# Kernel tuning notes

Hardware: AMD Instinct MI355X
Metric: run time of the kernel (lower is better)

## Reference

```python
import jax, jax.numpy as jnp
import numpy as np

TOP_K = 2

def setup_inputs() -> dict:
    key = jax.random.key(0)
    k1, k2, k3, k4 = jax.random.split(key, 4)
    B, S, H, E, F = 2, 1024, 1024, 16, 1024
    hidden_states = jax.random.normal(k1, (B, S, H), dtype=jnp.float32)
    router_w = jax.random.normal(k2, (H, E), dtype=jnp.float32) * 0.02
    w_gate_up = jax.random.normal(k3, (E, H, 2 * F), dtype=jnp.float32) * 0.02
    w_down = jax.random.normal(k4, (E, F, H), dtype=jnp.float32) * 0.02
    return {"hidden_states": hidden_states, "router_w": router_w,
            "w_gate_up": w_gate_up, "w_down": w_down}

def reference(hidden_states, router_w, w_gate_up, w_down):
    B, S, H = hidden_states.shape
    E = router_w.shape[-1]
    flat = hidden_states.reshape(-1, H)                      # [T, H]
    T = flat.shape[0]
    # Routing: topk_then_softmax (default softmax_order)
    logits = flat @ router_w                                 # [T, E]
    top_vals, top_idx = jax.lax.top_k(logits, TOP_K)         # [T, K]
    routing_weights = jax.nn.softmax(top_vals, axis=-1)      # [T, K]
    # Scatter routing weights into a dense combine matrix [T, E]
    combine = jnp.zeros((T, E), dtype=flat.dtype)
    combine = combine.at[jnp.arange(T)[:, None], top_idx].add(routing_weights)
    # Fused expert FFN (per _FusedExpertTemplate, act_fn = SiLU-gated)
    gu = jnp.einsum('th,ehf->etf', flat, w_gate_up)          # [E, T, 2F]
    gate, up = jnp.split(gu, 2, axis=-1)
    gated = jax.nn.silu(gate) * up                           # [E, T, F]
    expert_out = jnp.einsum('etf,efh->eth', gated, w_down)   # [E, T, H]
    out = jnp.einsum('eth,te->th', expert_out, combine)      # [T, H]
    return out.reshape(B, S, H)
```

## Files before the change

### kernel.cpp

```cpp
#include <hip/hip_runtime.h>

#define T_TOK 2048
#define H_DIM 1024
#define E_NUM 16
#define F_DIM 1024

typedef unsigned short u16;
typedef unsigned int u32;
typedef short s16x8 __attribute__((ext_vector_type(8)));
typedef float f32x4 __attribute__((ext_vector_type(4)));

__device__ __forceinline__ float b2f(u16 v) { return __uint_as_float(((u32)v) << 16); }
__device__ __forceinline__ u16 f2b(float f) {
  u32 u = __float_as_uint(f);
  return (u16)((u + 0x7fffu + ((u >> 16) & 1u)) >> 16);
}

__global__ void router_kernel(const float* __restrict__ hidden, const float* __restrict__ rw,
                              int* __restrict__ counts, int* __restrict__ routing_e,
                              float* __restrict__ routing_w) {
  int t = blockIdx.x;
  int lane = threadIdx.x;
  const float* xrow = hidden + (size_t)t * H_DIM;
  float acc[E_NUM];
#pragma unroll
  for (int e = 0; e < E_NUM; ++e) acc[e] = 0.f;
  for (int j = 0; j < H_DIM / 64; ++j) {
    int h = j * 64 + lane;
    float x = xrow[h];
    const float* wr = rw + h * E_NUM;
#pragma unroll
    for (int e = 0; e < E_NUM; ++e) acc[e] += x * wr[e];
  }
#pragma unroll
  for (int e = 0; e < E_NUM; ++e) {
    acc[e] += __shfl_xor(acc[e], 32, 64);
    acc[e] += __shfl_xor(acc[e], 16, 64);
    acc[e] += __shfl_xor(acc[e], 8, 64);
    acc[e] += __shfl_xor(acc[e], 4, 64);
    acc[e] += __shfl_xor(acc[e], 2, 64);
    acc[e] += __shfl_xor(acc[e], 1, 64);
  }
  if (lane == 0) {
    float v0 = -1e30f, v1 = -1e30f;
    int i0 = 0, i1 = 0;
#pragma unroll
    for (int e = 0; e < E_NUM; ++e) {
      float v = acc[e];
      if (v > v0) { v1 = v0; i1 = i0; v0 = v; i0 = e; }
      else if (v > v1) { v1 = v; i1 = e; }
    }
    float p0 = 1.f / (1.f + __expf(v1 - v0));
    routing_e[2 * t] = i0;
    routing_e[2 * t + 1] = i1;
    routing_w[2 * t] = p0;
    routing_w[2 * t + 1] = 1.f - p0;
    atomicAdd(&counts[i0], 1);
    atomicAdd(&counts[i1], 1);
  }
}

__global__ void scatter_kernel(const int* __restrict__ counts, int* __restrict__ offsets,
                               const int* __restrict__ routing_e, const float* __restrict__ routing_w,
                               int* __restrict__ token_of_slot, float* __restrict__ slot_w) {
  __shared__ int offs[E_NUM];
  __shared__ int cur[E_NUM];
  int tid = threadIdx.x;
  if (tid == 0) {
    int s = 0;
    for (int e = 0; e < E_NUM; ++e) { offs[e] = s; s += counts[e]; }
  }
  __syncthreads();
  if (tid < E_NUM) { offsets[tid] = offs[tid]; cur[tid] = offs[tid]; }
  __syncthreads();
  for (int i = tid; i < 2 * T_TOK; i += 256) {
    int e = routing_e[i];
    int pos = atomicAdd(&cur[e], 1);
    token_of_slot[pos] = i >> 1;
    slot_w[pos] = routing_w[i];
  }
}

struct f8v { float4 a, b; };

__device__ __forceinline__ void stage_w_pair(u32* __restrict__ B, int kp, int n0,
                                             const f8v& ev, const f8v& od) {
  const float* pe = (const float*)&ev;
  const float* po = (const float*)&od;
  int g0 = kp >> 2, w = kp & 3;
#pragma unroll
  for (int i = 0; i < 8; ++i) {
    int n = n0 + i;
    u32 word = (u32)f2b(pe[i]) | ((u32)f2b(po[i]) << 16);
    B[n * 16 + (((g0 ^ (n >> 3) ^ n) & 3) << 2) + w] = word;
  }
}

__device__ __forceinline__ s16x8 read_bfrag(const u32* __restrict__ B, int n, int q) {
  return *(const s16x8*)&B[n * 16 + (((q ^ (n >> 3) ^ n) & 3) << 2)];
}

__device__ __forceinline__ void split_pack(const float* __restrict__ p, uint4& hh, uint4& ll) {
  u16 h[8], l[8];
#pragma unroll
  for (int i = 0; i < 8; ++i) {
    h[i] = f2b(p[i]);
    l[i] = f2b(p[i] - b2f(h[i]));
  }
  hh.x = (u32)h[0] | ((u32)h[1] << 16);
  hh.y = (u32)h[2] | ((u32)h[3] << 16);
  hh.z = (u32)h[4] | ((u32)h[5] << 16);
  hh.w = (u32)h[6] | ((u32)h[7] << 16);
  ll.x = (u32)l[0] | ((u32)l[1] << 16);
  ll.y = (u32)l[2] | ((u32)l[3] << 16);
  ll.z = (u32)l[4] | ((u32)l[5] << 16);
  ll.w = (u32)l[6] | ((u32)l[7] << 16);
}

#define MFMA(a, b, c) __builtin_amdgcn_mfma_f32_16x16x32_bf16(a, b, c, 0, 0, 0)

__global__ __launch_bounds__(256, 2) void moe_gemm1(
    const float* __restrict__ hidden, const float* __restrict__ wgu,
    const int* __restrict__ token_of_slot, const int* __restrict__ counts,
    const int* __restrict__ offsets, float* __restrict__ act) {
  const int e = blockIdx.z;
  const int cnt = counts[e];
  const int m0 = blockIdx.y * 64;
  if (m0 >= cnt) return;
  const int off = offsets[e];
  const int f0 = blockIdx.x * 128;

  __shared__ u16 Xh[64][40];
  __shared__ u16 Xl[64][40];
  __shared__ u32 Bg[128 * 16];
  __shared__ u32 Bu[128 * 16];

  const int tid = threadIdx.x;
  const int lane = tid & 63;
  const int wave = tid >> 6;
  const int q = lane >> 4, ln = lane & 15;
  const int mb = (wave & 1) * 32, nb = (wave >> 1) * 64;

  const int xr = tid >> 2, xc = (tid & 3) * 8;
  const int tok = (m0 + xr < cnt) ? token_of_slot[off + m0 + xr] : 0;
  const float* xsrc = hidden + (size_t)tok * H_DIM + xc;

  const int kp = tid >> 4, n0 = (tid & 15) * 8;
  const float* wbase = wgu + (size_t)e * H_DIM * 2048;
  const float* wg0 = wbase + (size_t)(2 * kp) * 2048 + f0 + n0;
  const float* wu0 = wg0 + 1024;

  f32x4 zero = {0.f, 0.f, 0.f, 0.f};
  f32x4 accg[2][4], accu[2][4];
#pragma unroll
  for (int i = 0; i < 2; ++i)
#pragma unroll
    for (int j = 0; j < 4; ++j) { accg[i][j] = zero; accu[i][j] = zero; }

  for (int k0 = 0; k0 < H_DIM; k0 += 32) {
    float4 xa = *(const float4*)(xsrc + k0);
    float4 xb = *(const float4*)(xsrc + k0 + 4);
    size_t wofs = (size_t)k0 * 2048;
    f8v ge, go, ue, uo;
    ge.a = *(const float4*)(wg0 + wofs);
    ge.b = *(const float4*)(wg0 + wofs + 4);
    go.a = *(const float4*)(wg0 + wofs + 2048);
    go.b = *(const float4*)(wg0 + wofs + 2052);
    ue.a = *(const float4*)(wu0 + wofs);
    ue.b = *(const float4*)(wu0 + wofs + 4);
    uo.a = *(const float4*)(wu0 + wofs + 2048);
    uo.b = *(const float4*)(wu0 + wofs + 2052);
    __syncthreads();
    float xv[8] = {xa.x, xa.y, xa.z, xa.w, xb.x, xb.y, xb.z, xb.w};
    uint4 hh, ll;
    split_pack(xv, hh, ll);
    *(uint4*)&Xh[xr][xc] = hh;
    *(uint4*)&Xl[xr][xc] = ll;
    stage_w_pair(Bg, kp, n0, ge, go);
    stage_w_pair(Bu, kp, n0, ue, uo);
    __syncthreads();

    s16x8 ah[2], al[2];
    ah[0] = *(const s16x8*)&Xh[mb + ln][q * 8];
    ah[1] = *(const s16x8*)&Xh[mb + 16 + ln][q * 8];
    al[0] = *(const s16x8*)&Xl[mb + ln][q * 8];
    al[1] = *(const s16x8*)&Xl[mb + 16 + ln][q * 8];
#pragma unroll
    for (int j = 0; j < 4; ++j) {
      s16x8 bg = read_bfrag(Bg, nb + j * 16 + ln, q);
      s16x8 bu = read_bfrag(Bu, nb + j * 16 + ln, q);
#pragma unroll
      for (int i = 0; i < 2; ++i) {
        accg[i][j] = MFMA(ah[i], bg, accg[i][j]);
        accg[i][j] = MFMA(al[i], bg, accg[i][j]);
        accu[i][j] = MFMA(ah[i], bu, accu[i][j]);
        accu[i][j] = MFMA(al[i], bu, accu[i][j]);
      }
    }
  }

#pragma unroll
  for (int i = 0; i < 2; ++i) {
#pragma unroll
    for (int r = 0; r < 4; ++r) {
      int row = mb + i * 16 + q * 4 + r;
      if (m0 + row < cnt) {
        float* arow = act + (size_t)(off + m0 + row) * F_DIM + f0 + nb + ln;
#pragma unroll
        for (int j = 0; j < 4; ++j) {
          float g = accg[i][j][r], u = accu[i][j][r];
          arow[j * 16] = g * (1.f / (1.f + __expf(-g))) * u;
        }
      }
    }
  }
}

__global__ __launch_bounds__(256, 2) void moe_gemm2(
    const float* __restrict__ act, const float* __restrict__ wd,
    const int* __restrict__ token_of_slot, const float* __restrict__ slot_w,
    const int* __restrict__ counts, const int* __restrict__ offsets,
    float* __restrict__ out) {
  const int e = blockIdx.z;
  const int cnt = counts[e];
  const int m0 = blockIdx.y * 64;
  if (m0 >= cnt) return;
  const int off = offsets[e];
  const int h0 = blockIdx.x * 128;

  __shared__ u16 Ah[64][40];
  __shared__ u16 Al[64][40];
  __shared__ u32 Bd[128 * 16];

  const int tid = threadIdx.x;
  const int lane = tid & 63;
  const int wave = tid >> 6;
  const int q = lane >> 4, ln = lane & 15;
  const int mb = (wave & 1) * 32, nb = (wave >> 1) * 64;

  const int xr = tid >> 2, xc = (tid & 3) * 8;
  const int gs = (m0 + xr < cnt) ? (off + m0 + xr) : 0;
  const float* asrc = act + (size_t)gs * F_DIM + xc;

  const int kp = tid >> 4, n0 = (tid & 15) * 8;
  const float* wd0 = wd + (size_t)e * F_DIM * H_DIM + (size_t)(2 * kp) * H_DIM + h0 + n0;

  f32x4 zero = {0.f, 0.f, 0.f, 0.f};
  f32x4 acc[2][4];
#pragma unroll
  for (int i = 0; i < 2; ++i)
#pragma unroll
    for (int j = 0; j < 4; ++j) acc[i][j] = zero;

  for (int k0 = 0; k0 < F_DIM; k0 += 32) {
    float4 aa = *(const float4*)(asrc + k0);
    float4 ab = *(const float4*)(asrc + k0 + 4);
    size_t wofs = (size_t)k0 * H_DIM;
    f8v de, dd;
    de.a = *(const float4*)(wd0 + wofs);
    de.b = *(const float4*)(wd0 + wofs + 4);
    dd.a = *(const float4*)(wd0 + wofs + 1024);
    dd.b = *(const float4*)(wd0 + wofs + 1028);
    __syncthreads();
    float av[8] = {aa.x, aa.y, aa.z, aa.w, ab.x, ab.y, ab.z, ab.w};
    uint4 hh, ll;
    split_pack(av, hh, ll);
    *(uint4*)&Ah[xr][xc] = hh;
    *(uint4*)&Al[xr][xc] = ll;
    stage_w_pair(Bd, kp, n0, de, dd);
    __syncthreads();
    s16x8 ah[2], al[2];
    ah[0] = *(const s16x8*)&Ah[mb + ln][q * 8];
    ah[1] = *(const s16x8*)&Ah[mb + 16 + ln][q * 8];
    al[0] = *(const s16x8*)&Al[mb + ln][q * 8];
    al[1] = *(const s16x8*)&Al[mb + 16 + ln][q * 8];
#pragma unroll
    for (int j = 0; j < 4; ++j) {
      s16x8 bf = read_bfrag(Bd, nb + j * 16 + ln, q);
#pragma unroll
      for (int i = 0; i < 2; ++i) {
        acc[i][j] = MFMA(ah[i], bf, acc[i][j]);
        acc[i][j] = MFMA(al[i], bf, acc[i][j]);
      }
    }
  }
#pragma unroll
  for (int i = 0; i < 2; ++i) {
#pragma unroll
    for (int r = 0; r < 4; ++r) {
      int row = mb + i * 16 + q * 4 + r;
      if (m0 + row < cnt) {
        int slot = off + m0 + row;
        int tok = token_of_slot[slot];
        float wgt = slot_w[slot];
        float* orow = out + (size_t)tok * H_DIM + h0 + nb + ln;
#pragma unroll
        for (int j = 0; j < 4; ++j) atomicAdd(&orow[j * 16], wgt * acc[i][j][r]);
      }
    }
  }
}

extern "C" void kernel_launch(void* const* d_in, const int* in_sizes, int n_in,
                              void* d_out, int out_size, void* d_ws, size_t ws_size,
                              hipStream_t stream) {
  const float* hidden = (const float*)d_in[0];
  const float* rw = (const float*)d_in[1];
  const float* wgu = (const float*)d_in[2];
  const float* wd = (const float*)d_in[3];
  float* out = (float*)d_out;
  char* ws = (char*)d_ws;

  int* counts = (int*)(ws);
  int* offsets = (int*)(ws + 256);
  int* routing_e = (int*)(ws + 1024);
  float* routing_w = (float*)(ws + 17408);
  int* token_of_slot = (int*)(ws + 33792);
  float* slot_w = (float*)(ws + 50176);
  float* act = (float*)(ws + 131072);

  hipMemsetAsync(counts, 0, 64, stream);
  hipMemsetAsync(out, 0, (size_t)out_size * sizeof(float), stream);
  router_kernel<<<dim3(T_TOK), dim3(64), 0, stream>>>(hidden, rw, counts, routing_e, routing_w);
  scatter_kernel<<<dim3(1), dim3(256), 0, stream>>>(counts, offsets, routing_e, routing_w,
                                                    token_of_slot, slot_w);
  moe_gemm1<<<dim3(8, 32, E_NUM), dim3(256), 0, stream>>>(hidden, wgu, token_of_slot, counts,
                                                          offsets, act);
  moe_gemm2<<<dim3(8, 32, E_NUM), dim3(256), 0, stream>>>(act, wd, token_of_slot, slot_w, counts,
                                                          offsets, out);
}
```

Baseline: 430.4 us.

## Pre-convert weights and activations to bf16 tiles; double-buffer via global_load_lds

Adds prep kernels that convert the hidden states into bf16 hi/lo split arrays and repack the expert weights into swizzled bf16 tile layouts once per call. The GEMM kernels then stage weight tiles with asynchronous global_load_lds into double-buffered LDS and read the A fragments straight from global memory. The first GEMM also writes the activations as bf16 hi/lo pairs. This removes the per-iteration conversion work, halves the weight bytes the GEMMs read, and lets loads overlap compute, at the cost of extra full passes over the weights and a larger workspace.

```diff
diff --git a/kernel.cpp b/kernel.cpp
--- a/kernel.cpp
+++ b/kernel.cpp
@@ -4,6 +4,7 @@
 #define H_DIM 1024
 #define E_NUM 16
 #define F_DIM 1024
+#define NKB 32
 
 typedef unsigned short u16;
 typedef unsigned int u32;
@@ -14,6 +15,11 @@
 __device__ __forceinline__ u16 f2b(float f) {
   u32 u = __float_as_uint(f);
   return (u16)((u + 0x7fffu + ((u >> 16) & 1u)) >> 16);
+}
+
+__device__ __forceinline__ void gl_lds16(const u32* g, u32* l) {
+  __builtin_amdgcn_global_load_lds((const __attribute__((address_space(1))) void*)g,
+                                   (__attribute__((address_space(3))) void*)l, 16, 0, 0);
 }
 
 __global__ void router_kernel(const float* __restrict__ hidden, const float* __restrict__ rw,
@@ -81,25 +87,6 @@
   }
 }
 
-struct f8v { float4 a, b; };
-
-__device__ __forceinline__ void stage_w_pair(u32* __restrict__ B, int kp, int n0,
-                                             const f8v& ev, const f8v& od) {
-  const float* pe = (const float*)&ev;
-  const float* po = (const float*)&od;
-  int g0 = kp >> 2, w = kp & 3;
-#pragma unroll
-  for (int i = 0; i < 8; ++i) {
-    int n = n0 + i;
-    u32 word = (u32)f2b(pe[i]) | ((u32)f2b(po[i]) << 16);
-    B[n * 16 + (((g0 ^ (n >> 3) ^ n) & 3) << 2) + w] = word;
-  }
-}
-
-__device__ __forceinline__ s16x8 read_bfrag(const u32* __restrict__ B, int n, int q) {
-  return *(const s16x8*)&B[n * 16 + (((q ^ (n >> 3) ^ n) & 3) << 2)];
-}
-
 __device__ __forceinline__ void split_pack(const float* __restrict__ p, uint4& hh, uint4& ll) {
   u16 h[8], l[8];
 #pragma unroll
@@ -117,38 +104,87 @@
   ll.w = (u32)l[6] | ((u32)l[7] << 16);
 }
 
+__global__ __launch_bounds__(256) void prep_x(const float* __restrict__ x, u16* __restrict__ xh,
+                                              u16* __restrict__ xl) {
+  int i = blockIdx.x * 256 + threadIdx.x;
+  float4 a = ((const float4*)x)[2 * i];
+  float4 b = ((const float4*)x)[2 * i + 1];
+  float v[8] = {a.x, a.y, a.z, a.w, b.x, b.y, b.z, b.w};
+  uint4 hh, ll;
+  split_pack(v, hh, ll);
+  ((uint4*)xh)[i] = hh;
+  ((uint4*)xl)[i] = ll;
+}
+
+__global__ __launch_bounds__(256) void prep_w(const float* __restrict__ w, u32* __restrict__ wt,
+                                              int N) {
+  const int e = blockIdx.z, nbk = blockIdx.y, kb = blockIdx.x;
+  const float* src = w + (size_t)e * 1024 * N + (size_t)kb * 32 * N + nbk * 128;
+  u32* dst = wt + (((size_t)e * gridDim.y + nbk) * NKB + kb) * 2048;
+  __shared__ u16 L[32][132];
+  const int t = threadIdx.x;
+  const int kr = t >> 5;
+  const int nq = (t & 31) * 4;
+#pragma unroll
+  for (int p = 0; p < 4; ++p) {
+    int k = p * 8 + kr;
+    float4 v = *(const float4*)(src + (size_t)k * N + nq);
+    L[k][nq] = f2b(v.x);
+    L[k][nq + 1] = f2b(v.y);
+    L[k][nq + 2] = f2b(v.z);
+    L[k][nq + 3] = f2b(v.w);
+  }
+  __syncthreads();
+  const int n = t >> 1, half = t & 1;
+  const int s = ((n >> 3) ^ n) & 3;
+  __align__(16) u32 buf[8];
+#pragma unroll
+  for (int j = 0; j < 8; ++j) {
+    int pos = half * 8 + j;
+    int g0 = ((pos >> 2) ^ s) & 3;
+    int kp = g0 * 4 + (pos & 3);
+    buf[j] = (u32)L[2 * kp][n] | ((u32)L[2 * kp + 1][n] << 16);
+  }
+  *(uint4*)(dst + n * 16 + half * 8) = *(uint4*)&buf[0];
+  *(uint4*)(dst + n * 16 + half * 8 + 4) = *(uint4*)&buf[4];
+}
+
+__device__ __forceinline__ s16x8 read_bfrag(const u32* __restrict__ B, int n, int q) {
+  return *(const s16x8*)&B[n * 16 + (((q ^ (n >> 3) ^ n) & 3) << 2)];
+}
+
 #define MFMA(a, b, c) __builtin_amdgcn_mfma_f32_16x16x32_bf16(a, b, c, 0, 0, 0)
 
 __global__ __launch_bounds__(256, 2) void moe_gemm1(
-    const float* __restrict__ hidden, const float* __restrict__ wgu,
+    const u16* __restrict__ Xh, const u16* __restrict__ Xl, const u32* __restrict__ wgu_t,
     const int* __restrict__ token_of_slot, const int* __restrict__ counts,
-    const int* __restrict__ offsets, float* __restrict__ act) {
+    const int* __restrict__ offsets, u16* __restrict__ act_h, u16* __restrict__ act_l) {
   const int e = blockIdx.z;
   const int cnt = counts[e];
   const int m0 = blockIdx.y * 64;
   if (m0 >= cnt) return;
   const int off = offsets[e];
-  const int f0 = blockIdx.x * 128;
-
-  __shared__ u16 Xh[64][40];
-  __shared__ u16 Xl[64][40];
-  __shared__ u32 Bg[128 * 16];
-  __shared__ u32 Bu[128 * 16];
+  const int xb = blockIdx.x;
+
+  __shared__ u32 Bg[2][2048];
+  __shared__ u32 Bu[2][2048];
 
   const int tid = threadIdx.x;
   const int lane = tid & 63;
-  const int wave = tid >> 6;
+  const int wv = tid >> 6;
   const int q = lane >> 4, ln = lane & 15;
-  const int mb = (wave & 1) * 32, nb = (wave >> 1) * 64;
-
-  const int xr = tid >> 2, xc = (tid & 3) * 8;
-  const int tok = (m0 + xr < cnt) ? token_of_slot[off + m0 + xr] : 0;
-  const float* xsrc = hidden + (size_t)tok * H_DIM + xc;
-
-  const int kp = tid >> 4, n0 = (tid & 15) * 8;
-  const float* wbase = wgu + (size_t)e * H_DIM * 2048;
-  const float* wg0 = wbase + (size_t)(2 * kp) * 2048 + f0 + n0;
-  const float* wu0 = wg0 + 1024;
+  const int mb = (wv & 1) * 32, nb = (wv >> 1) * 64;
+
+  const int r0 = m0 + mb + ln, r1 = r0 + 16;
+  const int t0 = (r0 < cnt) ? token_of_slot[off + r0] : 0;
+  const int t1 = (r1 < cnt) ? token_of_slot[off + r1] : 0;
+  const u16* xh0 = Xh + (size_t)t0 * H_DIM + q * 8;
+  const u16* xh1 = Xh + (size_t)t1 * H_DIM + q * 8;
+  const u16* xl0 = Xl + (size_t)t0 * H_DIM + q * 8;
+  const u16* xl1 = Xl + (size_t)t1 * H_DIM + q * 8;
+
+  const u32* g_g = wgu_t + (((size_t)e * 16 + xb) * NKB) * 2048 + tid * 4;
+  const u32* g_u = wgu_t + (((size_t)e * 16 + xb + 8) * NKB) * 2048 + tid * 4;
 
   f32x4 zero = {0.f, 0.f, 0.f, 0.f};
   f32x4 accg[2][4], accu[2][4];
@@ -157,59 +193,64 @@
 #pragma unroll
     for (int j = 0; j < 4; ++j) { accg[i][j] = zero; accu[i][j] = zero; }
 
-  for (int k0 = 0; k0 < H_DIM; k0 += 32) {
-    float4 xa = *(const float4*)(xsrc + k0);
-    float4 xb = *(const float4*)(xsrc + k0 + 4);
-    size_t wofs = (size_t)k0 * 2048;
-    f8v ge, go, ue, uo;
-    ge.a = *(const float4*)(wg0 + wofs);
-    ge.b = *(const float4*)(wg0 + wofs + 4);
-    go.a = *(const float4*)(wg0 + wofs + 2048);
-    go.b = *(const float4*)(wg0 + wofs + 2052);
-    ue.a = *(const float4*)(wu0 + wofs);
-    ue.b = *(const float4*)(wu0 + wofs + 4);
-    uo.a = *(const float4*)(wu0 + wofs + 2048);
-    uo.b = *(const float4*)(wu0 + wofs + 2052);
-    __syncthreads();
-    float xv[8] = {xa.x, xa.y, xa.z, xa.w, xb.x, xb.y, xb.z, xb.w};
-    uint4 hh, ll;
-    split_pack(xv, hh, ll);
-    *(uint4*)&Xh[xr][xc] = hh;
-    *(uint4*)&Xl[xr][xc] = ll;
-    stage_w_pair(Bg, kp, n0, ge, go);
-    stage_w_pair(Bu, kp, n0, ue, uo);
-    __syncthreads();
-
-    s16x8 ah[2], al[2];
-    ah[0] = *(const s16x8*)&Xh[mb + ln][q * 8];
-    ah[1] = *(const s16x8*)&Xh[mb + 16 + ln][q * 8];
-    al[0] = *(const s16x8*)&Xl[mb + ln][q * 8];
-    al[1] = *(const s16x8*)&Xl[mb + 16 + ln][q * 8];
-#pragma unroll
-    for (int j = 0; j < 4; ++j) {
-      s16x8 bg = read_bfrag(Bg, nb + j * 16 + ln, q);
-      s16x8 bu = read_bfrag(Bu, nb + j * 16 + ln, q);
-#pragma unroll
-      for (int i = 0; i < 2; ++i) {
-        accg[i][j] = MFMA(ah[i], bg, accg[i][j]);
-        accg[i][j] = MFMA(al[i], bg, accg[i][j]);
-        accu[i][j] = MFMA(ah[i], bu, accu[i][j]);
-        accu[i][j] = MFMA(al[i], bu, accu[i][j]);
-      }
-    }
-  }
-
+#define STAGE1(kbn, LG, LU)                          \
+  {                                                  \
+    const u32* sg = g_g + (size_t)(kbn) * 2048;      \
+    const u32* su = g_u + (size_t)(kbn) * 2048;      \
+    gl_lds16(sg, (LG) + wv * 256);                   \
+    gl_lds16(sg + 1024, (LG) + 1024 + wv * 256);     \
+    gl_lds16(su, (LU) + wv * 256);                   \
+    gl_lds16(su + 1024, (LU) + 1024 + wv * 256);     \
+  }
+
+  STAGE1(0, &Bg[0][0], &Bu[0][0]);
+  __syncthreads();
+
+#define G1BODY(kb, CG, CU, NG, NU)                               \
+  {                                                              \
+    const int koff = (kb) * 32;                                  \
+    s16x8 ah0 = *(const s16x8*)(xh0 + koff);                     \
+    s16x8 ah1 = *(const s16x8*)(xh1 + koff);                     \
+    s16x8 al0 = *(const s16x8*)(xl0 + koff);                     \
+    s16x8 al1 = *(const s16x8*)(xl1 + koff);                     \
+    if ((kb) + 1 < NKB) STAGE1((kb) + 1, NG, NU);                \
+    _Pragma("unroll")                                            \
+    for (int j = 0; j < 4; ++j) {                                \
+      s16x8 bg = read_bfrag(CG, nb + j * 16 + ln, q);            \
+      s16x8 bu = read_bfrag(CU, nb + j * 16 + ln, q);            \
+      accg[0][j] = MFMA(ah0, bg, accg[0][j]);                    \
+      accg[1][j] = MFMA(ah1, bg, accg[1][j]);                    \
+      accu[0][j] = MFMA(ah0, bu, accu[0][j]);                    \
+      accu[1][j] = MFMA(ah1, bu, accu[1][j]);                    \
+      accg[0][j] = MFMA(al0, bg, accg[0][j]);                    \
+      accg[1][j] = MFMA(al1, bg, accg[1][j]);                    \
+      accu[0][j] = MFMA(al0, bu, accu[0][j]);                    \
+      accu[1][j] = MFMA(al1, bu, accu[1][j]);                    \
+    }                                                            \
+    __syncthreads();                                             \
+  }
+
+  for (int kb = 0; kb < NKB; kb += 2) {
+    G1BODY(kb, &Bg[0][0], &Bu[0][0], &Bg[1][0], &Bu[1][0]);
+    G1BODY(kb + 1, &Bg[1][0], &Bu[1][0], &Bg[0][0], &Bu[0][0]);
+  }
+
+  const int bcol = xb * 128 + nb + ln;
 #pragma unroll
   for (int i = 0; i < 2; ++i) {
 #pragma unroll
     for (int r = 0; r < 4; ++r) {
       int row = mb + i * 16 + q * 4 + r;
       if (m0 + row < cnt) {
-        float* arow = act + (size_t)(off + m0 + row) * F_DIM + f0 + nb + ln;
+        size_t rb = (size_t)(off + m0 + row) * F_DIM + bcol;
 #pragma unroll
         for (int j = 0; j < 4; ++j) {
           float g = accg[i][j][r], u = accu[i][j][r];
-          arow[j * 16] = g * (1.f / (1.f + __expf(-g))) * u;
+          float a = g * (1.f / (1.f + __expf(-g))) * u;
+          u16 h = f2b(a);
+          u16 l = f2b(a - b2f(h));
+          act_h[rb + j * 16] = h;
+          act_l[rb + j * 16] = l;
         }
       }
     }
@@ -217,7 +258,7 @@
 }
 
 __global__ __launch_bounds__(256, 2) void moe_gemm2(
-    const float* __restrict__ act, const float* __restrict__ wd,
+    const u16* __restrict__ Ah, const u16* __restrict__ Al, const u32* __restrict__ wd_t,
     const int* __restrict__ token_of_slot, const float* __restrict__ slot_w,
     const int* __restrict__ counts, const int* __restrict__ offsets,
     float* __restrict__ out) {
@@ -226,24 +267,25 @@
   const int m0 = blockIdx.y * 64;
   if (m0 >= cnt) return;
   const int off = offsets[e];
-  const int h0 = blockIdx.x * 128;
-
-  __shared__ u16 Ah[64][40];
-  __shared__ u16 Al[64][40];
-  __shared__ u32 Bd[128 * 16];
+  const int xb = blockIdx.x;
+
+  __shared__ u32 Bd[2][2048];
 
   const int tid = threadIdx.x;
   const int lane = tid & 63;
-  const int wave = tid >> 6;
+  const int wv = tid >> 6;
   const int q = lane >> 4, ln = lane & 15;
-  const int mb = (wave & 1) * 32, nb = (wave >> 1) * 64;
-
-  const int xr = tid >> 2, xc = (tid & 3) * 8;
-  const int gs = (m0 + xr < cnt) ? (off + m0 + xr) : 0;
-  const float* asrc = act + (size_t)gs * F_DIM + xc;
-
-  const int kp = tid >> 4, n0 = (tid & 15) * 8;
-  const float* wd0 = wd + (size_t)e * F_DIM * H_DIM + (size_t)(2 * kp) * H_DIM + h0 + n0;
+  const int mb = (wv & 1) * 32, nb = (wv >> 1) * 64;
+
+  const int r0 = m0 + mb + ln, r1 = r0 + 16;
+  const int s0 = off + ((r0 < cnt) ? r0 : 0);
+  const int s1 = off + ((r1 < cnt) ? r1 : 0);
+  const u16* ah0 = Ah + (size_t)s0 * F_DIM + q * 8;
+  const u16* ah1 = Ah + (size_t)s1 * F_DIM + q * 8;
+  const u16* al0 = Al + (size_t)s0 * F_DIM + q * 8;
+  const u16* al1 = Al + (size_t)s1 * F_DIM + q * 8;
+
+  const u32* g_d = wd_t + (((size_t)e * 8 + xb) * NKB) * 2048 + tid * 4;
 
   f32x4 zero = {0.f, 0.f, 0.f, 0.f};
   f32x4 acc[2][4];
@@ -252,38 +294,40 @@
 #pragma unroll
     for (int j = 0; j < 4; ++j) acc[i][j] = zero;
 
-  for (int k0 = 0; k0 < F_DIM; k0 += 32) {
-    float4 aa = *(const float4*)(asrc + k0);
-    float4 ab = *(const float4*)(asrc + k0 + 4);
-    size_t wofs = (size_t)k0 * H_DIM;
-    f8v de, dd;
-    de.a = *(const float4*)(wd0 + wofs);
-    de.b = *(const float4*)(wd0 + wofs + 4);
-    dd.a = *(const float4*)(wd0 + wofs + 1024);
-    dd.b = *(const float4*)(wd0 + wofs + 1028);
-    __syncthreads();
-    float av[8] = {aa.x, aa.y, aa.z, aa.w, ab.x, ab.y, ab.z, ab.w};
-    uint4 hh, ll;
-    split_pack(av, hh, ll);
-    *(uint4*)&Ah[xr][xc] = hh;
-    *(uint4*)&Al[xr][xc] = ll;
-    stage_w_pair(Bd, kp, n0, de, dd);
-    __syncthreads();
-    s16x8 ah[2], al[2];
-    ah[0] = *(const s16x8*)&Ah[mb + ln][q * 8];
-    ah[1] = *(const s16x8*)&Ah[mb + 16 + ln][q * 8];
-    al[0] = *(const s16x8*)&Al[mb + ln][q * 8];
-    al[1] = *(const s16x8*)&Al[mb + 16 + ln][q * 8];
-#pragma unroll
-    for (int j = 0; j < 4; ++j) {
-      s16x8 bf = read_bfrag(Bd, nb + j * 16 + ln, q);
-#pragma unroll
-      for (int i = 0; i < 2; ++i) {
-        acc[i][j] = MFMA(ah[i], bf, acc[i][j]);
-        acc[i][j] = MFMA(al[i], bf, acc[i][j]);
-      }
-    }
-  }
+#define STAGE2(kbn, LD)                              \
+  {                                                  \
+    const u32* sd = g_d + (size_t)(kbn) * 2048;      \
+    gl_lds16(sd, (LD) + wv * 256);                   \
+    gl_lds16(sd + 1024, (LD) + 1024 + wv * 256);     \
+  }
+
+  STAGE2(0, &Bd[0][0]);
+  __syncthreads();
+
+#define G2BODY(kb, CD, ND)                               \
+  {                                                      \
+    const int koff = (kb) * 32;                          \
+    s16x8 a0 = *(const s16x8*)(ah0 + koff);              \
+    s16x8 a1 = *(const s16x8*)(ah1 + koff);              \
+    s16x8 b0 = *(const s16x8*)(al0 + koff);              \
+    s16x8 b1 = *(const s16x8*)(al1 + koff);              \
+    if ((kb) + 1 < NKB) STAGE2((kb) + 1, ND);            \
+    _Pragma("unroll")                                    \
+    for (int j = 0; j < 4; ++j) {                        \
+      s16x8 bf = read_bfrag(CD, nb + j * 16 + ln, q);    \
+      acc[0][j] = MFMA(a0, bf, acc[0][j]);               \
+      acc[1][j] = MFMA(a1, bf, acc[1][j]);               \
+      acc[0][j] = MFMA(b0, bf, acc[0][j]);               \
+      acc[1][j] = MFMA(b1, bf, acc[1][j]);               \
+    }                                                    \
+    __syncthreads();                                     \
+  }
+
+  for (int kb = 0; kb < NKB; kb += 2) {
+    G2BODY(kb, &Bd[0][0], &Bd[1][0]);
+    G2BODY(kb + 1, &Bd[1][0], &Bd[0][0]);
+  }
+
 #pragma unroll
   for (int i = 0; i < 2; ++i) {
 #pragma unroll
@@ -293,7 +337,7 @@
         int slot = off + m0 + row;
         int tok = token_of_slot[slot];
         float wgt = slot_w[slot];
-        float* orow = out + (size_t)tok * H_DIM + h0 + nb + ln;
+        float* orow = out + (size_t)tok * H_DIM + xb * 128 + nb + ln;
 #pragma unroll
         for (int j = 0; j < 4; ++j) atomicAdd(&orow[j * 16], wgt * acc[i][j][r]);
       }
@@ -317,15 +361,23 @@
   float* routing_w = (float*)(ws + 17408);
   int* token_of_slot = (int*)(ws + 33792);
   float* slot_w = (float*)(ws + 50176);
-  float* act = (float*)(ws + 131072);
+  u16* Xh = (u16*)(ws + 131072ull);
+  u16* Xl = (u16*)(ws + 4325376ull);
+  u16* act_h = (u16*)(ws + 8519680ull);
+  u16* act_l = (u16*)(ws + 16908288ull);
+  u32* wgu_t = (u32*)(ws + 25296896ull);
+  u32* wd_t  = (u32*)(ws + 92405760ull);
 
   hipMemsetAsync(counts, 0, 64, stream);
   hipMemsetAsync(out, 0, (size_t)out_size * sizeof(float), stream);
   router_kernel<<<dim3(T_TOK), dim3(64), 0, stream>>>(hidden, rw, counts, routing_e, routing_w);
   scatter_kernel<<<dim3(1), dim3(256), 0, stream>>>(counts, offsets, routing_e, routing_w,
                                                     token_of_slot, slot_w);
-  moe_gemm1<<<dim3(8, 32, E_NUM), dim3(256), 0, stream>>>(hidden, wgu, token_of_slot, counts,
-                                                          offsets, act);
-  moe_gemm2<<<dim3(8, 32, E_NUM), dim3(256), 0, stream>>>(act, wd, token_of_slot, slot_w, counts,
-                                                          offsets, out);
-}
+  prep_x<<<dim3(T_TOK * H_DIM / 8 / 256), dim3(256), 0, stream>>>(hidden, Xh, Xl);
+  prep_w<<<dim3(NKB, 16, E_NUM), dim3(256), 0, stream>>>(wgu, wgu_t, 2048);
+  prep_w<<<dim3(NKB, 8, E_NUM), dim3(256), 0, stream>>>(wd, wd_t, 1024);
+  moe_gemm1<<<dim3(8, 32, E_NUM), dim3(256), 0, stream>>>(Xh, Xl, wgu_t, token_of_slot, counts,
+                                                          offsets, act_h, act_l);
+  moe_gemm2<<<dim3(8, 32, E_NUM), dim3(256), 0, stream>>>(act_h, act_l, wd_t, token_of_slot,
+                                                          slot_w, counts, offsets, out);
+}
```

After: 479.9 us. 11.5% more time.
